# Optimization experiments

Measured on AMD Instinct MI355X. Metric: run time of the kernel, lower is better.

The kernel has to match this reference:

```python
import jax, jax.numpy as jnp
from jax import lax
import numpy as np

HID = 128            # hidden_dim
DILS = (1, 3, 9, 27) # dilations (used only by the dense dilated convs)
CONV_SIZE = 3        # dilated conv kernel size
KER = 3              # LVC kernel size
SLOPE = 0.2          # lReLU slope after preconv
BLOCK_SLOPE = float(KER)  # NOTE: source passes ker_size into LVC_ConvBlock's slope arg
COND = 512           # cond channels


def setup_inputs() -> dict:
    key = jax.random.key(0)
    ks = jax.random.split(key, 12)
    B, T, Lc = 4, 32768, 128  # hop_size = T // Lc = 256
    nl = len(DILS)
    f = lambda k, s: jax.random.normal(k, s, dtype=jnp.float32) * 0.02
    return {
        "x": jax.random.normal(ks[0], (B, 1, T), dtype=jnp.float32),
        "c": jax.random.normal(ks[1], (B, COND, Lc), dtype=jnp.float32),
        # KernelPredictor 1x1 convs (weight-normed at init == plain weights)
        "kernel_w": f(ks[2], (HID * HID * KER * nl, COND)),
        "kernel_b": f(ks[3], (HID * HID * KER * nl,)),
        "biasp_w": f(ks[4], (HID * nl, COND)),
        "biasp_b": f(ks[5], (HID * nl,)),
        "pre_w": f(ks[6], (HID, 1)),
        "pre_b": f(ks[7], (HID,)),
        "block_w": f(ks[8], (nl, HID, HID, CONV_SIZE)),
        "block_b": f(ks[9], (nl, HID)),
        "post_w": f(ks[10], (1, HID)),
        "post_b": f(ks[11], (1,)),
    }


def _leaky(x, s):
    return jnp.where(x >= 0, x, s * x)


def _conv1x1(x, w, b):  # x: (B,C,T), w: (O,C), b: (O,)
    return jnp.einsum('oc,bct->bot', w, x) + b[:, None]


def _dilconv(x, w, b, d):  # x: (B,C,T), w: (O,I,K)
    pad = d * (CONV_SIZE - 1) // 2
    y = lax.conv_general_dilated(x, w, window_strides=(1,), padding=[(pad, pad)],
                                 rhs_dilation=(d,), dimension_numbers=('NCH', 'OIH', 'NCH'))
    return y + b[:, None]


def _lvc(x, kernel, bias, hop):
    # x: (B,C,T); kernel: (B,C,O,K,L); bias: (B,O,L). dilation=1 (as in source call).
    B, C, T = x.shape
    O, K, L = kernel.shape[2], kernel.shape[3], kernel.shape[4]
    p = (K - 1) // 2
    xp = jnp.pad(x, ((0, 0), (0, 0), (p, p)))
    # stride-1 sliding windows of width K, grouped into L hop-blocks of size hop
    win = jnp.stack([xp[:, :, j:j + T] for j in range(K)], axis=-1)  # (B,C,T,K)
    win = win.reshape(B, C, L, hop, K)
    o = jnp.einsum('bilsk,biokl->bols', win, kernel) + bias[:, :, :, None]
    return o.reshape(B, O, T)


def reference(x, c, kernel_w, kernel_b, biasp_w, biasp_b, pre_w, pre_b,
              block_w, block_b, post_w, post_b):
    B, _, T = x.shape
    Lc = c.shape[-1]
    nl = len(DILS)
    hop = T // Lc
    # kernel predictor: view order (B, layers, in, out, K, L)
    k_all = _conv1x1(c, kernel_w, kernel_b).reshape(B, nl, HID, HID, KER, Lc)
    b_all = _conv1x1(c, biasp_w, biasp_b).reshape(B, nl, HID, Lc)
    h = _leaky(_conv1x1(x, pre_w, pre_b), SLOPE)
    for i, d in enumerate(DILS):
        h = _lvc(h, k_all[:, i], b_all[:, i], hop)
        h = _leaky(h, BLOCK_SLOPE)
        h = _dilconv(h, block_w[i], block_b[i], d)
        h = _leaky(h, BLOCK_SLOPE)
    return _conv1x1(h, post_w, post_b)
```

## Files before the change

kernel.cpp:

```cpp
#include <hip/hip_runtime.h>

#define T_LEN 32768
#define HIDC  128
#define LC    128
#define HOP   256
#define CONDC 512
#define NLAY  4
#define MROWS 49152

typedef __attribute__((ext_vector_type(8))) short short8;
typedef __attribute__((ext_vector_type(4))) float f32x4;

static __device__ __forceinline__ unsigned short f2b(float f) {
  union { float f; unsigned u; } v; v.f = f;
  unsigned r = v.u + 0x7FFFu + ((v.u >> 16) & 1u);
  return (unsigned short)(r >> 16);
}
static __device__ __forceinline__ float b2f(unsigned short h) {
  union { unsigned u; float f; } v; v.u = ((unsigned)h) << 16;
  return v.f;
}


__global__ void k_cbt(const float* __restrict__ c, unsigned short* __restrict__ cbt) {
  int idx = blockIdx.x * 256 + threadIdx.x;
  int n = idx >> 9, ch = idx & 511;
  int b = n >> 7, l = n & 127;
  cbt[idx] = f2b(c[(size_t)(b * CONDC + ch) * LC + l]);
}

__global__ void k_bwt(const float* __restrict__ bw, unsigned short* __restrict__ bwt) {
  int idx = blockIdx.x * 256 + threadIdx.x;
  int o = idx & 127, i = (idx >> 7) & 127, kk = idx >> 14;
  int k = kk % 3, layer = kk / 3;
  bwt[idx] = f2b(bw[(size_t)((layer * HIDC + o) * HIDC + i) * 3 + k]);
}

__global__ void k_bias(const float* __restrict__ c, const float* __restrict__ bw,
                       const float* __restrict__ bb, float* __restrict__ ball) {
  int m = blockIdx.x, b = blockIdx.y, l = threadIdx.x;
  const float* crow = c + (size_t)b * CONDC * LC + l;
  const float* wrow = bw + (size_t)m * CONDC;
  float acc = 0.f;
  for (int ch = 0; ch < CONDC; ++ch) acc = fmaf(wrow[ch], crow[(size_t)ch * LC], acc);
  int layer = m >> 7, o = m & 127;
  ball[((size_t)(b * NLAY + layer) * HIDC + o) * LC + l] = acc + bb[m];
}

__global__ void k_pre(const float* __restrict__ x, const float* __restrict__ pw,
                      const float* __restrict__ pb, unsigned short* __restrict__ h) {
  int idx = blockIdx.x * 256 + threadIdx.x;
  int o4 = (idx & 31) << 2;
  int bt = idx >> 5;
  float xv = x[bt];
  float4 w = *(const float4*)(pw + o4);
  float4 bi = *(const float4*)(pb + o4);
  float r0 = fmaf(w.x, xv, bi.x); r0 = r0 >= 0.f ? r0 : 0.2f * r0;
  float r1 = fmaf(w.y, xv, bi.y); r1 = r1 >= 0.f ? r1 : 0.2f * r1;
  float r2 = fmaf(w.z, xv, bi.z); r2 = r2 >= 0.f ? r2 : 0.2f * r2;
  float r3 = fmaf(w.w, xv, bi.w); r3 = r3 >= 0.f ? r3 : 0.2f * r3;
  ushort4 s; s.x = f2b(r0); s.y = f2b(r1); s.z = f2b(r2); s.w = f2b(r3);
  *(ushort4*)(h + (size_t)bt * HIDC + o4) = s;
}

__global__ void k_post(const unsigned short* __restrict__ h, const float* __restrict__ pw,
                       const float* __restrict__ pb, float* __restrict__ out) {
  int t = blockIdx.x * 256 + threadIdx.x;
  const unsigned short* r = h + (size_t)t * HIDC;
  float acc = 0.f;
#pragma unroll
  for (int o = 0; o < HIDC; o += 8) {
    int4 w = *(const int4*)(r + o);
    int ws_[4] = {w.x, w.y, w.z, w.w};
#pragma unroll
    for (int j = 0; j < 4; ++j) {
      unsigned v = (unsigned)ws_[j];
      acc = fmaf(b2f((unsigned short)(v & 0xFFFFu)), pw[o + j * 2], acc);
      acc = fmaf(b2f((unsigned short)(v >> 16)),     pw[o + j * 2 + 1], acc);
    }
  }
  out[t] = acc + pb[0];
}

__global__ __launch_bounds__(256) void k_kpred(
    const float* __restrict__ A, const float* __restrict__ bias,
    const unsigned short* __restrict__ Bt, unsigned short* __restrict__ C) {
  __shared__ __align__(16) unsigned short As[128 * 72];
  __shared__ __align__(16) unsigned short Bs[128 * 72];
  const int mtile = blockIdx.x * 128;
  const int ntile = blockIdx.y * 128;
  const int tid = threadIdx.x;
  const int wave = tid >> 6, lane = tid & 63;
  const int wm = (wave & 1) * 64, wn = (wave >> 1) * 64;
  const int lm = lane & 15, quad = lane >> 4;
  f32x4 acc[4][4] = {};
  for (int k0 = 0; k0 < CONDC; k0 += 64) {
#pragma unroll
    for (int it = 0; it < 8; ++it) {
      int idx = it * 256 + tid;
      int row = idx >> 4, kq = (idx & 15) << 2;
      float4 v = *(const float4*)(A + (size_t)(mtile + row) * CONDC + k0 + kq);
      ushort4 s; s.x = f2b(v.x); s.y = f2b(v.y); s.z = f2b(v.z); s.w = f2b(v.w);
      *(ushort4*)(&As[row * 72 + kq]) = s;
    }
#pragma unroll
    for (int it = 0; it < 4; ++it) {
      int idx = it * 256 + tid;
      int row = idx >> 3, k8 = (idx & 7) << 3;
      *(int4*)(&Bs[row * 72 + k8]) = *(const int4*)(Bt + (size_t)(ntile + row) * CONDC + k0 + k8);
    }
    __syncthreads();
#pragma unroll
    for (int kk = 0; kk < 2; ++kk) {
      short8 af[4], bf[4];
#pragma unroll
      for (int mb = 0; mb < 4; ++mb)
        af[mb] = *(const short8*)(&As[(wm + mb * 16 + lm) * 72 + kk * 32 + quad * 8]);
#pragma unroll
      for (int nb = 0; nb < 4; ++nb)
        bf[nb] = *(const short8*)(&Bs[(wn + nb * 16 + lm) * 72 + kk * 32 + quad * 8]);
#pragma unroll
      for (int mb = 0; mb < 4; ++mb)
#pragma unroll
        for (int nb = 0; nb < 4; ++nb)
          acc[mb][nb] = __builtin_amdgcn_mfma_f32_16x16x32_bf16(af[mb], bf[nb], acc[mb][nb], 0, 0, 0);
    }
    __syncthreads();
  }
#pragma unroll
  for (int mb = 0; mb < 4; ++mb) {
    int m0 = mtile + wm + mb * 16 + quad * 4;
    float b0 = bias[m0], b1 = bias[m0 + 1], b2 = bias[m0 + 2], b3 = bias[m0 + 3];
#pragma unroll
    for (int nb = 0; nb < 4; ++nb) {
      int n = ntile + wn + nb * 16 + lm;
      f32x4 v = acc[mb][nb];
      ushort4 s;
      s.x = f2b(v.x + b0); s.y = f2b(v.y + b1); s.z = f2b(v.z + b2); s.w = f2b(v.w + b3);
      *(ushort4*)(&C[(size_t)n * MROWS + m0]) = s;
    }
  }
}

__global__ __launch_bounds__(512) void k_lvc(
    const unsigned short* __restrict__ hin, const unsigned short* __restrict__ kbuf,
    const float* __restrict__ ball, unsigned short* __restrict__ hout, int layer) {
  __shared__ __align__(16) unsigned short Hs[258 * 40];
  __shared__ __align__(16) unsigned short As[3 * 128 * 40];
  const int l = blockIdx.x, b = blockIdx.y;
  const int t0 = l * HOP;
  const int tid = threadIdx.x;
  const int wave = tid >> 6, lane = tid & 63;
  const int wm = (wave & 1) * 64, wn = (wave >> 1) * 64;
  const int lm = lane & 15, quad = lane >> 4;
  const unsigned short* hb = hin + (size_t)b * T_LEN * HIDC;
  const unsigned short* kb = kbuf + (size_t)(b * LC + l) * MROWS;
  f32x4 acc[4][4] = {};
  for (int ic = 0; ic < HIDC; ic += 32) {
    __syncthreads();
#pragma unroll
    for (int p = 0; p < 5; ++p) {
      int idx = p * 512 + tid;
      if (idx < 258 * 8) {
        int u = idx >> 3, i4 = (idx & 7) << 2;
        int t = t0 + u - 1;
        ushort4 v; v.x = v.y = v.z = v.w = 0;
        if (t >= 0 && t < T_LEN) v = *(const ushort4*)(hb + (size_t)t * HIDC + ic + i4);
        *(ushort4*)(&Hs[u * 40 + i4]) = v;
      }
    }
#pragma unroll
    for (int p = 0; p < 24; ++p) {
      int idx = p * 512 + tid;
      int o = idx & 127, ii = (idx >> 7) & 31, k = idx >> 12;
      As[(k * 128 + o) * 40 + ii] = kb[((size_t)(ic + ii) * HIDC + o) * 3 + k];
    }
    __syncthreads();
#pragma unroll
    for (int k = 0; k < 3; ++k) {
      short8 af[4], bf[4];
#pragma unroll
      for (int mb = 0; mb < 4; ++mb)
        af[mb] = *(const short8*)(&As[(k * 128 + wm + mb * 16 + lm) * 40 + quad * 8]);
#pragma unroll
      for (int nb = 0; nb < 4; ++nb)
        bf[nb] = *(const short8*)(&Hs[(wn + nb * 16 + lm + k) * 40 + quad * 8]);
#pragma unroll
      for (int mb = 0; mb < 4; ++mb)
#pragma unroll
        for (int nb = 0; nb < 4; ++nb)
          acc[mb][nb] = __builtin_amdgcn_mfma_f32_16x16x32_bf16(af[mb], bf[nb], acc[mb][nb], 0, 0, 0);
    }
  }
  const float* bp = ball + (size_t)(b * NLAY + layer) * HIDC * LC + l;
#pragma unroll
  for (int mb = 0; mb < 4; ++mb) {
    int o0 = wm + mb * 16 + quad * 4;
    float bi[4];
#pragma unroll
    for (int j = 0; j < 4; ++j) bi[j] = bp[(size_t)(o0 + j) * LC];
#pragma unroll
    for (int nb = 0; nb < 4; ++nb) {
      int s = wn + nb * 16 + lm;
      f32x4 v = acc[mb][nb];
      float r0 = v.x + bi[0]; r0 = r0 >= 0.f ? r0 : 3.f * r0;
      float r1 = v.y + bi[1]; r1 = r1 >= 0.f ? r1 : 3.f * r1;
      float r2 = v.z + bi[2]; r2 = r2 >= 0.f ? r2 : 3.f * r2;
      float r3 = v.w + bi[3]; r3 = r3 >= 0.f ? r3 : 3.f * r3;
      ushort4 st; st.x = f2b(r0); st.y = f2b(r1); st.z = f2b(r2); st.w = f2b(r3);
      *(ushort4*)(&hout[((size_t)b * T_LEN + t0 + s) * HIDC + o0]) = st;
    }
  }
}

__global__ __launch_bounds__(512) void k_dconv(
    const unsigned short* __restrict__ hin, const unsigned short* __restrict__ bwt,
    const float* __restrict__ bb, unsigned short* __restrict__ hout, int d) {
  __shared__ __align__(16) unsigned short Hs[310 * 40];
  __shared__ __align__(16) unsigned short As[3 * 128 * 40];
  const int tb = blockIdx.x * HOP, b = blockIdx.y;
  const int U8 = (HOP + 2 * d) * 8;
  const int tid = threadIdx.x;
  const int wave = tid >> 6, lane = tid & 63;
  const int wm = (wave & 1) * 64, wn = (wave >> 1) * 64;
  const int lm = lane & 15, quad = lane >> 4;
  const unsigned short* hb = hin + (size_t)b * T_LEN * HIDC;
  f32x4 acc[4][4] = {};
  for (int ic = 0; ic < HIDC; ic += 32) {
    __syncthreads();
#pragma unroll
    for (int p = 0; p < 5; ++p) {
      int idx = p * 512 + tid;
      if (idx < U8) {
        int u = idx >> 3, i4 = (idx & 7) << 2;
        int t = tb + u - d;
        ushort4 v; v.x = v.y = v.z = v.w = 0;
        if (t >= 0 && t < T_LEN) v = *(const ushort4*)(hb + (size_t)t * HIDC + ic + i4);
        *(ushort4*)(&Hs[u * 40 + i4]) = v;
      }
    }
#pragma unroll
    for (int p = 0; p < 24; ++p) {
      int idx = p * 512 + tid;
      int o = idx & 127, ii = (idx >> 7) & 31, k = idx >> 12;
      As[(k * 128 + o) * 40 + ii] = bwt[(size_t)(k * HIDC + ic + ii) * HIDC + o];
    }
    __syncthreads();
#pragma unroll
    for (int k = 0; k < 3; ++k) {
      short8 af[4], bf[4];
#pragma unroll
      for (int mb = 0; mb < 4; ++mb)
        af[mb] = *(const short8*)(&As[(k * 128 + wm + mb * 16 + lm) * 40 + quad * 8]);
#pragma unroll
      for (int nb = 0; nb < 4; ++nb)
        bf[nb] = *(const short8*)(&Hs[(wn + nb * 16 + lm + k * d) * 40 + quad * 8]);
#pragma unroll
      for (int mb = 0; mb < 4; ++mb)
#pragma unroll
        for (int nb = 0; nb < 4; ++nb)
          acc[mb][nb] = __builtin_amdgcn_mfma_f32_16x16x32_bf16(af[mb], bf[nb], acc[mb][nb], 0, 0, 0);
    }
  }
#pragma unroll
  for (int mb = 0; mb < 4; ++mb) {
    int o0 = wm + mb * 16 + quad * 4;
    float bi[4];
#pragma unroll
    for (int j = 0; j < 4; ++j) bi[j] = bb[o0 + j];
#pragma unroll
    for (int nb = 0; nb < 4; ++nb) {
      int s = wn + nb * 16 + lm;
      f32x4 v = acc[mb][nb];
      float r0 = v.x + bi[0]; r0 = r0 >= 0.f ? r0 : 3.f * r0;
      float r1 = v.y + bi[1]; r1 = r1 >= 0.f ? r1 : 3.f * r1;
      float r2 = v.z + bi[2]; r2 = r2 >= 0.f ? r2 : 3.f * r2;
      float r3 = v.w + bi[3]; r3 = r3 >= 0.f ? r3 : 3.f * r3;
      ushort4 st; st.x = f2b(r0); st.y = f2b(r1); st.z = f2b(r2); st.w = f2b(r3);
      *(ushort4*)(&hout[((size_t)b * T_LEN + tb + s) * HIDC + o0]) = st;
    }
  }
}

extern "C" void kernel_launch(void* const* d_in, const int* in_sizes, int n_in,
                              void* d_out, int out_size, void* d_ws, size_t ws_size,
                              hipStream_t stream) {
  const float* x        = (const float*)d_in[0];
  const float* c        = (const float*)d_in[1];
  const float* kernel_w = (const float*)d_in[2];
  const float* kernel_b = (const float*)d_in[3];
  const float* biasp_w  = (const float*)d_in[4];
  const float* biasp_b  = (const float*)d_in[5];
  const float* pre_w    = (const float*)d_in[6];
  const float* pre_b    = (const float*)d_in[7];
  const float* block_w  = (const float*)d_in[8];
  const float* block_b  = (const float*)d_in[9];
  const float* post_w   = (const float*)d_in[10];
  const float* post_b   = (const float*)d_in[11];
  float* out = (float*)d_out;

  char* ws = (char*)d_ws;
  unsigned short* h0   = (unsigned short*)ws;
  unsigned short* h1   = (unsigned short*)(ws + 33554432);
  unsigned short* kbuf = (unsigned short*)(ws + 67108864);
  float*          ball = (float*)(ws + 117440512);
  unsigned short* cbt  = (unsigned short*)(ws + 118489088);
  unsigned short* bwt  = (unsigned short*)(ws + 119013376);

  k_cbt<<<1024, 256, 0, stream>>>(c, cbt);
  k_bwt<<<768, 256, 0, stream>>>(block_w, bwt);
  k_bias<<<dim3(512, 4), 128, 0, stream>>>(c, biasp_w, biasp_b, ball);
  k_pre<<<16384, 256, 0, stream>>>(x, pre_w, pre_b, h0);

  unsigned short* cur = h0;
  unsigned short* nxt = h1;
  const int dils[4] = {1, 3, 9, 27};
  for (int layer = 0; layer < 4; ++layer) {
    k_kpred<<<dim3(384, 4), 256, 0, stream>>>(kernel_w + (size_t)layer * MROWS * CONDC,
                                              kernel_b + (size_t)layer * MROWS, cbt, kbuf);
    k_lvc<<<dim3(128, 4), 512, 0, stream>>>(cur, kbuf, ball, nxt, layer);
    unsigned short* t = cur; cur = nxt; nxt = t;
    k_dconv<<<dim3(128, 4), 512, 0, stream>>>(cur, bwt + (size_t)layer * 3 * HIDC * HIDC,
                                              block_b + layer * HIDC, nxt, dils[layer]);
    t = cur; cur = nxt; nxt = t;
  }
  k_post<<<512, 256, 0, stream>>>(cur, post_w, post_b, out);
}
```

Baseline: 1.085 ms.

## Reorder predicted kernels and conv weights so LDS staging uses 16-byte loads

The kernel-predictor GEMM now permutes its output rows so each (k, o) pair stores a contiguous run over input channels, and the block conv weights are transposed to the same [k][o][i] order. The LVC and dilated-conv kernels can then fill their weight tiles with int4 vector loads instead of 24 strided scalar gathers per thread, and the activation tiles also switch from 8-byte to 16-byte loads. This targets the uncoalesced global-memory traffic in the staging loops. In exchange, the predictor GEMM reads its A rows with a stride of 384 rows, which may hurt that kernel's locality.

```diff
diff --git a/kernel.cpp b/kernel.cpp
--- a/kernel.cpp
+++ b/kernel.cpp
@@ -31,9 +31,9 @@
 
 __global__ void k_bwt(const float* __restrict__ bw, unsigned short* __restrict__ bwt) {
   int idx = blockIdx.x * 256 + threadIdx.x;
-  int o = idx & 127, i = (idx >> 7) & 127, kk = idx >> 14;
-  int k = kk % 3, layer = kk / 3;
-  bwt[idx] = f2b(bw[(size_t)((layer * HIDC + o) * HIDC + i) * 3 + k]);
+  int i = idx & 127, o = (idx >> 7) & 127, kl = idx >> 14;
+  int k = kl % 3, layer = kl / 3;
+  bwt[idx] = f2b(bw[((size_t)(layer * HIDC + o) * HIDC + i) * 3 + k]);
 }
 
 __global__ void k_bias(const float* __restrict__ c, const float* __restrict__ bw,
@@ -88,6 +88,7 @@
   __shared__ __align__(16) unsigned short As[128 * 72];
   __shared__ __align__(16) unsigned short Bs[128 * 72];
   const int mtile = blockIdx.x * 128;
+  const int oc = (blockIdx.x & 127) * 3 + (blockIdx.x >> 7);
   const int ntile = blockIdx.y * 128;
   const int tid = threadIdx.x;
   const int wave = tid >> 6, lane = tid & 63;
@@ -99,7 +100,7 @@
     for (int it = 0; it < 8; ++it) {
       int idx = it * 256 + tid;
       int row = idx >> 4, kq = (idx & 15) << 2;
-      float4 v = *(const float4*)(A + (size_t)(mtile + row) * CONDC + k0 + kq);
+      float4 v = *(const float4*)(A + ((size_t)row * 384 + oc) * CONDC + k0 + kq);
       ushort4 s; s.x = f2b(v.x); s.y = f2b(v.y); s.z = f2b(v.z); s.w = f2b(v.w);
       *(ushort4*)(&As[row * 72 + kq]) = s;
     }
@@ -129,8 +130,12 @@
   }
 #pragma unroll
   for (int mb = 0; mb < 4; ++mb) {
-    int m0 = mtile + wm + mb * 16 + quad * 4;
-    float b0 = bias[m0], b1 = bias[m0 + 1], b2 = bias[m0 + 2], b3 = bias[m0 + 3];
+    int i0 = wm + mb * 16 + quad * 4;
+    int m0 = mtile + i0;
+    float b0 = bias[(size_t)i0 * 384 + oc];
+    float b1 = bias[(size_t)(i0 + 1) * 384 + oc];
+    float b2 = bias[(size_t)(i0 + 2) * 384 + oc];
+    float b3 = bias[(size_t)(i0 + 3) * 384 + oc];
 #pragma unroll
     for (int nb = 0; nb < 4; ++nb) {
       int n = ntile + wn + nb * 16 + lm;
@@ -159,21 +164,21 @@
   for (int ic = 0; ic < HIDC; ic += 32) {
     __syncthreads();
 #pragma unroll
-    for (int p = 0; p < 5; ++p) {
+    for (int p = 0; p < 3; ++p) {
       int idx = p * 512 + tid;
-      if (idx < 258 * 8) {
-        int u = idx >> 3, i4 = (idx & 7) << 2;
+      if (idx < 258 * 4) {
+        int u = idx >> 2, i8 = (idx & 3) << 3;
         int t = t0 + u - 1;
-        ushort4 v; v.x = v.y = v.z = v.w = 0;
-        if (t >= 0 && t < T_LEN) v = *(const ushort4*)(hb + (size_t)t * HIDC + ic + i4);
-        *(ushort4*)(&Hs[u * 40 + i4]) = v;
+        int4 v = {0, 0, 0, 0};
+        if (t >= 0 && t < T_LEN) v = *(const int4*)(hb + (size_t)t * HIDC + ic + i8);
+        *(int4*)(&Hs[u * 40 + i8]) = v;
       }
     }
 #pragma unroll
-    for (int p = 0; p < 24; ++p) {
+    for (int p = 0; p < 3; ++p) {
       int idx = p * 512 + tid;
-      int o = idx & 127, ii = (idx >> 7) & 31, k = idx >> 12;
-      As[(k * 128 + o) * 40 + ii] = kb[((size_t)(ic + ii) * HIDC + o) * 3 + k];
+      int ko = idx >> 2, i8 = (idx & 3) << 3;
+      *(int4*)(&As[ko * 40 + i8]) = *(const int4*)(kb + (size_t)ko * HIDC + ic + i8);
     }
     __syncthreads();
 #pragma unroll
@@ -219,7 +224,7 @@
   __shared__ __align__(16) unsigned short Hs[310 * 40];
   __shared__ __align__(16) unsigned short As[3 * 128 * 40];
   const int tb = blockIdx.x * HOP, b = blockIdx.y;
-  const int U8 = (HOP + 2 * d) * 8;
+  const int U4 = (HOP + 2 * d) * 4;
   const int tid = threadIdx.x;
   const int wave = tid >> 6, lane = tid & 63;
   const int wm = (wave & 1) * 64, wn = (wave >> 1) * 64;
@@ -229,21 +234,21 @@
   for (int ic = 0; ic < HIDC; ic += 32) {
     __syncthreads();
 #pragma unroll
-    for (int p = 0; p < 5; ++p) {
+    for (int p = 0; p < 3; ++p) {
       int idx = p * 512 + tid;
-      if (idx < U8) {
-        int u = idx >> 3, i4 = (idx & 7) << 2;
+      if (idx < U4) {
+        int u = idx >> 2, i8 = (idx & 3) << 3;
         int t = tb + u - d;
-        ushort4 v; v.x = v.y = v.z = v.w = 0;
-        if (t >= 0 && t < T_LEN) v = *(const ushort4*)(hb + (size_t)t * HIDC + ic + i4);
-        *(ushort4*)(&Hs[u * 40 + i4]) = v;
+        int4 v = {0, 0, 0, 0};
+        if (t >= 0 && t < T_LEN) v = *(const int4*)(hb + (size_t)t * HIDC + ic + i8);
+        *(int4*)(&Hs[u * 40 + i8]) = v;
       }
     }
 #pragma unroll
-    for (int p = 0; p < 24; ++p) {
+    for (int p = 0; p < 3; ++p) {
       int idx = p * 512 + tid;
-      int o = idx & 127, ii = (idx >> 7) & 31, k = idx >> 12;
-      As[(k * 128 + o) * 40 + ii] = bwt[(size_t)(k * HIDC + ic + ii) * HIDC + o];
+      int ko = idx >> 2, i8 = (idx & 3) << 3;
+      *(int4*)(&As[ko * 40 + i8]) = *(const int4*)(bwt + (size_t)ko * HIDC + ic + i8);
     }
     __syncthreads();
 #pragma unroll
```

After: 1.051 ms. 1.03x faster.
